# Performance work log

Measured on AMD Instinct MI355X. Metric: run time of the kernel, lower is better.

Reference implementation:

```python
import jax, jax.numpy as jnp
import numpy as np

B, L, D, H = 2, 2048, 1024, 16
HD = D // H
EPS = 1e-6

def _rms(x, w):
    return x * jax.lax.rsqrt(jnp.mean(x * x, axis=-1, keepdims=True) + EPS) * w

def _lin(x, w, b=None):
    y = x @ w.T
    return y if b is None else y + b

def setup_inputs() -> dict:
    key = jax.random.key(0)
    ks = jax.random.split(key, 16)
    def w(i, shape, s=0.02):
        return jax.random.normal(ks[i], shape, dtype=jnp.float32) * s
    return dict(
        z=jax.random.normal(ks[0], (B, L, D), dtype=jnp.float32),
        connection=jax.random.normal(ks[1], (B, L, D), dtype=jnp.float32),
        w_z=jnp.ones(D, jnp.float32), w_c=jnp.ones(D, jnp.float32), w_mlp=jnp.ones(D, jnp.float32),
        f_w1=w(2, (2 * D, D)), f_b1=jnp.zeros(2 * D, jnp.float32),
        f_w2=w(3, (D, 2 * D)), f_b2=jnp.zeros(D, jnp.float32),
        g_w1=w(4, (D, 2 * D)), g_b1=jnp.zeros(D, jnp.float32),
        g_w2=w(5, (D, D)), g_b2=jnp.zeros(D, jnp.float32),
        dt=jnp.float32(0.1),
        q_w=w(6, (D, 2 * D)), k_w=w(7, (D, 2 * D)), v_w=w(8, (D, D)), o_w=w(9, (D, D)),
        temp=jnp.float32(1.0),
        cu_w1=w(10, (2 * D, 3 * D)), cu_b1=jnp.zeros(2 * D, jnp.float32),
        cu_w2=w(11, (D, 2 * D)), cu_b2=jnp.zeros(D, jnp.float32),
        m_w1=w(12, (4 * D, D)), m_b1=jnp.zeros(4 * D, jnp.float32),
        m_w2=w(13, (D, 4 * D)), m_b2=jnp.zeros(D, jnp.float32),
    )

def reference(z, connection, w_z, w_c, w_mlp,
              f_w1, f_b1, f_w2, f_b2, g_w1, g_b1, g_w2, g_b2, dt,
              q_w, k_w, v_w, o_w, temp,
              cu_w1, cu_b1, cu_w2, cu_b2,
              m_w1, m_b1, m_w2, m_b2):
    z_before = z
    zn = _rms(z, w_z)
    cn = _rms(connection, w_c)

    # covariant vector field: dz = dt * (F(zn) + gamma(cat(cn, F(zn))))
    dz_local = _lin(jax.nn.silu(_lin(zn, f_w1, f_b1)), f_w2, f_b2)
    corr = _lin(jnp.tanh(_lin(jnp.concatenate([cn, dz_local], -1), g_w1, g_b1)), g_w2, g_b2)
    dz = dt * (dz_local + corr)

    # covariant sigmoid attention
    zc = jnp.concatenate([zn, cn], -1)                       # [B,L,2D]
    Q = _lin(zc, q_w).reshape(B, L, H, HD).transpose(0, 2, 1, 3)  # bhld
    K = _lin(zc, k_w).reshape(B, L, H, HD).transpose(0, 2, 1, 3)
    V = _lin(zn, v_w).reshape(B, L, H, HD).transpose(0, 2, 1, 3)
    scores = jnp.einsum('bhld,bhmd->bhlm', Q, K) * (HD ** -0.5) * temp
    rel = jax.nn.sigmoid(scores)
    rel_sum = jnp.clip(jnp.sum(rel, -1, keepdims=True), 1.0, None)
    attn = jnp.einsum('bhlm,bhmd->bhld', rel, V) / rel_sum
    ctx = _lin(attn.transpose(0, 2, 1, 3).reshape(B, L, D), o_w)

    z1 = z + dz + ctx

    # connection update
    delta = _lin(jax.nn.silu(_lin(jnp.concatenate([connection, z1, dz], -1), cu_w1, cu_b1)), cu_w2, cu_b2)
    conn_new = connection + delta

    # MLP block
    z2 = z1 + _lin(jax.nn.silu(_lin(_rms(z1, w_mlp), m_w1, m_b1)), m_w2, m_b2)
    return (z2, conn_new, z_before)
```

## Files before the change

### kernel.cpp

```cpp
#include <hip/hip_runtime.h>


typedef unsigned short u16;
typedef __attribute__((ext_vector_type(8))) short short8;
typedef __attribute__((ext_vector_type(8))) unsigned short us8;
typedef __attribute__((ext_vector_type(4))) float f32x4;
typedef __attribute__((ext_vector_type(4))) unsigned short us4;
typedef __attribute__((ext_vector_type(2))) unsigned int u32x2;

__device__ __forceinline__ float b2f(u16 u) {
    union { unsigned u; float f; } c; c.u = ((unsigned)u) << 16; return c.f;
}
__device__ __forceinline__ u16 f2b(float f) {
    union { float f; unsigned u; } c; c.f = f;
    unsigned x = c.u;
    unsigned r = (x + 0x7fffu + ((x >> 16) & 1u)) >> 16;
    return (u16)r;
}
__device__ __forceinline__ float fast_rcp(float x) {
    return __builtin_amdgcn_rcpf(x);
}
__device__ __forceinline__ unsigned cvt_pk_bf16(float a, float b) {
    unsigned r;
    asm("v_cvt_pk_bf16_f32 %0, %1, %2" : "=v"(r) : "v"(a), "v"(b));
    return r;
}

__device__ __forceinline__ void async_copy16(const u16* g, u16* l) {
    __builtin_amdgcn_global_load_lds(
        (const __attribute__((address_space(1))) unsigned int*)(g),
        (__attribute__((address_space(3))) unsigned int*)(l), 16, 0, 0);
}

__global__ __launch_bounds__(256) void cvt_k(const float* __restrict__ s,
                                             u16* __restrict__ d, int n) {
    int i = (blockIdx.x * 256 + threadIdx.x) * 4;
    if (i >= n) return;
    f32x4 v = *(const f32x4*)(s + i);
    us4 o;
#pragma unroll
    for (int k = 0; k < 4; k++) o[k] = f2b(v[k]);
    *(us4*)(d + i) = o;
}

__global__ __launch_bounds__(256) void rmsf_k(const float* __restrict__ x,
                                              const float* __restrict__ w,
                                              u16* __restrict__ y,
                                              float* __restrict__ cp,
                                              u16* __restrict__ cb, int D) {
    int n = blockIdx.x;
    const float* xr = x + (size_t)n * D;
    int i0 = threadIdx.x << 2;
    f32x4 v = *(const f32x4*)(xr + i0);
    if (cp) *(f32x4*)(cp + (size_t)n * D + i0) = v;
    if (cb) {
        us4 o2;
#pragma unroll
        for (int k = 0; k < 4; k++) o2[k] = f2b(v[k]);
        *(us4*)(cb + (size_t)n * D + i0) = o2;
    }
    float s = v[0] * v[0] + v[1] * v[1] + v[2] * v[2] + v[3] * v[3];
#pragma unroll
    for (int m = 32; m >= 1; m >>= 1) s += __shfl_xor(s, m, 64);
    __shared__ float red[4];
    if ((threadIdx.x & 63) == 0) red[threadIdx.x >> 6] = s;
    __syncthreads();
    float tot = red[0] + red[1] + red[2] + red[3];
    float scale = rsqrtf(tot / (float)D + 1e-6f);
    f32x4 wv = *(const f32x4*)(w + i0);
    us4 o;
#pragma unroll
    for (int k = 0; k < 4; k++) o[k] = f2b(v[k] * scale * wv[k]);
    *(us4*)(y + (size_t)n * D + i0) = o;
}

__global__ __launch_bounds__(256) void rmsb_k(const u16* __restrict__ x,
                                              const float* __restrict__ w,
                                              u16* __restrict__ y, int D) {
    int n = blockIdx.x;
    const u16* xr = x + (size_t)n * D;
    int i0 = threadIdx.x << 2;
    us4 xv = *(const us4*)(xr + i0);
    float v[4]; float s = 0.f;
#pragma unroll
    for (int k = 0; k < 4; k++) { v[k] = b2f(xv[k]); s += v[k] * v[k]; }
#pragma unroll
    for (int m = 32; m >= 1; m >>= 1) s += __shfl_xor(s, m, 64);
    __shared__ float red[4];
    if ((threadIdx.x & 63) == 0) red[threadIdx.x >> 6] = s;
    __syncthreads();
    float tot = red[0] + red[1] + red[2] + red[3];
    float scale = rsqrtf(tot / (float)D + 1e-6f);
    f32x4 wv = *(const f32x4*)(w + i0);
    us4 o;
#pragma unroll
    for (int k = 0; k < 4; k++) o[k] = f2b(v[k] * scale * wv[k]);
    *(us4*)(y + (size_t)n * D + i0) = o;
}

template <int BM, int BN, int NSEG>
__global__ __launch_bounds__(256) void gemm_t(const u16* __restrict__ A0,
                                              const u16* __restrict__ A1,
                                              const u16* __restrict__ A2,
                                              const u16* __restrict__ W,
                                              const float* __restrict__ bias,
                                              u16* __restrict__ C,
                                              const u16* __restrict__ Eb,
                                              const float* __restrict__ Ef,
                                              const float* __restrict__ sc,
                                              float* __restrict__ Cf,
                                              int K, int O, int act, int mode) {
    constexpr int WM = BM / 2, WN = BN / 2;
    constexpr int NI = WM / 16, NJ = WN / 16;
    __shared__ u16 Asm[2][BM * 64];
    __shared__ u16 Bsm[2][BN * 64];

    const int tid = threadIdx.x;
    const int wid = tid >> 6, lane = tid & 63;
    const int l15 = lane & 15, quad = lane >> 4;
    const int lsw = l15 & 7;

    const int nwg = gridDim.x * gridDim.y;
    int id = blockIdx.y * gridDim.x + blockIdx.x;
    id = (id & 7) * (nwg >> 3) + (id >> 3);
    const int bx = id % gridDim.x, by = id / gridDim.x;

    const int row0 = by * BM, col0 = bx * BN;
    const int wm = (wid >> 1) * WM, wn = (wid & 1) * WN;

    const int rb = tid >> 3;
    const int gg = ((tid & 7) ^ (rb & 7)) << 3;
    const int sA = (NSEG == 1) ? K : 1024;
    const size_t aoff = (size_t)(row0 + rb) * sA + gg;
    const size_t boff = (size_t)(col0 + rb) * K + gg;
    const int ldsb = wid << 9;

    f32x4 acc[NI][NJ];
#pragma unroll
    for (int i = 0; i < NI; i++)
#pragma unroll
        for (int j = 0; j < NJ; j++) acc[i][j] = (f32x4){0.f, 0.f, 0.f, 0.f};

    auto stage = [&](int buf, int kof) {
        const u16* Ab; int kcol;
        if constexpr (NSEG == 1) { Ab = A0; kcol = kof; }
        else {
            int seg = kof >> 10;
            Ab = (seg == 0) ? A0 : ((NSEG == 3 && seg == 2) ? A2 : A1);
            kcol = kof & 1023;
        }
        const u16* as = Ab + aoff + kcol;
        const u16* bs = W + boff + kof;
#pragma unroll
        for (int i = 0; i < BM / 32; i++)
            async_copy16(as + (size_t)(32 * i) * sA, &Asm[buf][(i << 11) + ldsb]);
#pragma unroll
        for (int i = 0; i < BN / 32; i++)
            async_copy16(bs + (size_t)(32 * i) * K, &Bsm[buf][(i << 11) + ldsb]);
    };

    const int nk = K >> 6;
    stage(0, 0);
    __syncthreads();
    for (int kk = 0; kk < nk; kk++) {
        int cur = kk & 1;
        if (kk + 1 < nk) stage(1 - cur, (kk + 1) << 6);
        const u16* Ab = Asm[cur];
        const u16* Bb = Bsm[cur];
#pragma unroll
        for (int h = 0; h < 2; h++) {
            const int gq = (((h << 2) + quad) ^ lsw) << 3;
            short8 af[NI], bf[NJ];
#pragma unroll
            for (int i = 0; i < NI; i++)
                af[i] = *(const short8*)&Ab[(wm + i * 16 + l15) * 64 + gq];
#pragma unroll
            for (int j = 0; j < NJ; j++)
                bf[j] = *(const short8*)&Bb[(wn + j * 16 + l15) * 64 + gq];
#pragma unroll
            for (int i = 0; i < NI; i++)
#pragma unroll
                for (int j = 0; j < NJ; j++)
                    acc[i][j] = __builtin_amdgcn_mfma_f32_16x16x32_bf16(af[i], bf[j], acc[i][j], 0, 0, 0);
        }
        __syncthreads();
    }

    if (mode == 1) {
#pragma unroll
        for (int j = 0; j < NJ; j++) {
            int col = col0 + wn + j * 16 + l15;
            int h = col >> 6, d = col & 63;
#pragma unroll
            for (int i = 0; i < NI; i++) {
                int rowb = row0 + wm + i * 16 + (quad << 2);
                int bb_ = rowb >> 11;
                int tok = rowb & 2047;
                u32x2 pk2;
                pk2[0] = cvt_pk_bf16(acc[i][j][0], acc[i][j][1]);
                pk2[1] = cvt_pk_bf16(acc[i][j][2], acc[i][j][3]);
                *(u32x2*)&C[(size_t)(((bb_ << 4) + h) * 64 + d) * 2048 + tok] = pk2;
            }
        }
    } else {
        float dtv = (mode == 2) ? sc[0] : 0.f;
#pragma unroll
        for (int j = 0; j < NJ; j++) {
            int col = col0 + wn + j * 16 + l15;
            float bb = bias ? bias[col] : 0.f;
#pragma unroll
            for (int i = 0; i < NI; i++) {
                int rowb = row0 + wm + i * 16 + (quad << 2);
#pragma unroll
                for (int g = 0; g < 4; g++) {
                    float v = acc[i][j][g] + bb;
                    if (act == 1) {
                        v = v * fast_rcp(1.f + __expf(-v));
                    } else if (act == 2) {
                        float t = __expf(v * 2.f);
                        v = 1.f - 2.f * fast_rcp(1.f + t);
                    }
                    size_t idx = (size_t)(rowb + g) * O + col;
                    if (mode == 0)      C[idx] = f2b(v);
                    else if (mode == 2) C[idx] = f2b(dtv * (b2f(Eb[idx]) + v));
                    else if (mode == 3) C[idx] = f2b(Ef[idx] + b2f(Eb[idx]) + v);
                    else if (mode == 4) Cf[idx] = Ef[idx] + v;
                    else                Cf[idx] = b2f(Eb[idx]) + v;
                }
            }
        }
    }
}

__global__ __launch_bounds__(256) void attn_k(const u16* __restrict__ QK,
                                              const u16* __restrict__ VT,
                                              const float* __restrict__ temp_p,
                                              u16* __restrict__ Oa) {
    const int L = 2048, D = 1024, SQ = 2048;
    __shared__ u16 Ks[2][64 * 64];
    __shared__ u16 Vs[2][64 * 64];
    __shared__ u16 plds[4][16 * 72];

    const int tid = threadIdx.x;
    const int w = tid >> 6, lane = tid & 63;
    const int l15 = lane & 15, quad = lane >> 4;
    int id = blockIdx.x;
    id = (id & 7) * 64 + (id >> 3);
    const int bh = id >> 4;
    const int qb0 = (id & 15) << 7;
    const int b = bh >> 4, h = bh & 15;
    const float nsc2 = -0.125f * temp_p[0] * 1.44269504f;

    short8 aq[2][2];
#pragma unroll
    for (int qt = 0; qt < 2; qt++) {
        size_t row = (size_t)(b * L + qb0 + w * 32 + qt * 16 + l15) * SQ + h * 64;
#pragma unroll
        for (int hf = 0; hf < 2; hf++)
            aq[qt][hf] = *(const short8*)(QK + row + hf * 32 + quad * 8);
    }

    const u16* Kbase = QK + 1024 + (size_t)(b * L) * SQ + h * 64;
    const u16* VTb   = VT + (size_t)bh * 64 * L;

    const int i0 = tid, i1 = tid + 256;
    const int r0 = i0 >> 3, g0 = (i0 & 7) ^ (r0 & 7);
    const int r1 = i1 >> 3, g1 = (i1 & 7) ^ (r1 & 7);
    const u16* kS0 = Kbase + (size_t)r0 * SQ + g0 * 8;
    const u16* kS1 = Kbase + (size_t)r1 * SQ + g1 * 8;
    const u16* vS0 = VTb + (size_t)r0 * L + g0 * 8;
    const u16* vS1 = VTb + (size_t)r1 * L + g1 * 8;

    auto stage = [&](int buf, int mc) {
        async_copy16(kS0 + (size_t)mc * SQ, &Ks[buf][w << 9]);
        async_copy16(kS1 + (size_t)mc * SQ, &Ks[buf][2048 + (w << 9)]);
        async_copy16(vS0 + mc, &Vs[buf][w << 9]);
        async_copy16(vS1 + mc, &Vs[buf][2048 + (w << 9)]);
    };

    f32x4 acc[2][4];
#pragma unroll
    for (int i = 0; i < 2; i++)
#pragma unroll
        for (int j = 0; j < 4; j++) acc[i][j] = (f32x4){0.f, 0.f, 0.f, 0.f};
    float rs[2] = {0.f, 0.f};
    u16* P = plds[w];
    const int lsw = l15 & 7;

    stage(0, 0);
    __syncthreads();
    for (int it = 0; it < 32; it++) {
        int cur = it & 1;
        if (it < 31) stage(1 - cur, (it + 1) << 6);
        const u16* Kt = Ks[cur];
        const u16* Vt = Vs[cur];
#pragma unroll
        for (int qt = 0; qt < 2; qt++) {
#pragma unroll
            for (int ks = 0; ks < 4; ks++) {
                f32x4 s = (f32x4){0.f, 0.f, 0.f, 0.f};
#pragma unroll
                for (int hf = 0; hf < 2; hf++) {
                    int slot = ((ks * 16 + l15) * 8 + ((hf * 4 + quad) ^ lsw)) * 8;
                    short8 bk = *(const short8*)&Kt[slot];
                    s = __builtin_amdgcn_mfma_f32_16x16x32_bf16(bk, aq[qt][hf], s, 0, 0, 0);
                }
                float p0 = fast_rcp(1.f + __builtin_amdgcn_exp2f(s[0] * nsc2));
                float p1 = fast_rcp(1.f + __builtin_amdgcn_exp2f(s[1] * nsc2));
                float p2 = fast_rcp(1.f + __builtin_amdgcn_exp2f(s[2] * nsc2));
                float p3 = fast_rcp(1.f + __builtin_amdgcn_exp2f(s[3] * nsc2));
                rs[qt] += (p0 + p1) + (p2 + p3);
                u32x2 pk2;
                pk2[0] = cvt_pk_bf16(p0, p1);
                pk2[1] = cvt_pk_bf16(p2, p3);
                *(u32x2*)&P[l15 * 72 + ks * 16 + (quad << 2)] = pk2;
            }
#pragma unroll
            for (int kh = 0; kh < 2; kh++) {
                short8 ap = *(const short8*)&P[l15 * 72 + kh * 32 + quad * 8];
#pragma unroll
                for (int dt = 0; dt < 4; dt++) {
                    int slot = ((dt * 16 + l15) * 8 + ((kh * 4 + quad) ^ lsw)) * 8;
                    short8 bv = *(const short8*)&Vt[slot];
                    acc[qt][dt] = __builtin_amdgcn_mfma_f32_16x16x32_bf16(ap, bv, acc[qt][dt], 0, 0, 0);
                }
            }
        }
        __syncthreads();
    }

#pragma unroll
    for (int qt = 0; qt < 2; qt++) {
        rs[qt] += __shfl_xor(rs[qt], 16, 64);
        rs[qt] += __shfl_xor(rs[qt], 32, 64);
    }

#pragma unroll
    for (int qt = 0; qt < 2; qt++) {
        u16* orow = Oa + (size_t)(b * L + qb0 + w * 32 + qt * 16) * D + h * 64;
#pragma unroll
        for (int g = 0; g < 4; g++) {
            int row = quad * 4 + g;
            float denom = __shfl(rs[qt], row, 64);
            float rd = fast_rcp(fmaxf(denom, 1.0f));
#pragma unroll
            for (int dt = 0; dt < 4; dt++)
                orow[(size_t)row * D + dt * 16 + l15] = f2b(acc[qt][dt][g] * rd);
        }
    }
}

extern "C" void kernel_launch(void* const* d_in, const int* in_sizes, int n_in,
                              void* d_out, int out_size, void* d_ws, size_t ws_size,
                              hipStream_t stream) {
    const int B = 2, L = 2048, D = 1024, H = 16, N = B * L;
    const float* z      = (const float*)d_in[0];
    const float* conn   = (const float*)d_in[1];
    const float* w_z    = (const float*)d_in[2];
    const float* w_c    = (const float*)d_in[3];
    const float* w_mlp  = (const float*)d_in[4];
    const float* f_w1   = (const float*)d_in[5];
    const float* f_b1   = (const float*)d_in[6];
    const float* f_w2   = (const float*)d_in[7];
    const float* f_b2   = (const float*)d_in[8];
    const float* g_w1   = (const float*)d_in[9];
    const float* g_b1   = (const float*)d_in[10];
    const float* g_w2   = (const float*)d_in[11];
    const float* g_b2   = (const float*)d_in[12];
    const float* dt_p   = (const float*)d_in[13];
    const float* q_w    = (const float*)d_in[14];
    const float* k_w    = (const float*)d_in[15];
    const float* v_w    = (const float*)d_in[16];
    const float* o_w    = (const float*)d_in[17];
    const float* temp_p = (const float*)d_in[18];
    const float* cu_w1  = (const float*)d_in[19];
    const float* cu_b1  = (const float*)d_in[20];
    const float* cu_w2  = (const float*)d_in[21];
    const float* cu_b2  = (const float*)d_in[22];
    const float* m_w1   = (const float*)d_in[23];
    const float* m_b1   = (const float*)d_in[24];
    const float* m_w2   = (const float*)d_in[25];
    const float* m_b2   = (const float*)d_in[26];

    float* out = (float*)d_out;
    u16* ws  = (u16*)d_ws;
    const size_t U = (size_t)N * D;

    u16* zn    = ws + 0 * U;
    u16* cn    = ws + 1 * U;
    u16* h1    = ws + 2 * U;
    u16* dzl   = ws + 4 * U;
    u16* gh    = ws + 5 * U;
    u16* dz    = ws + 6 * U;
    u16* connb = ws + 7 * U;
    u16* QK    = ws + 2 * U;
    u16* VT    = ws + 4 * U;
    u16* attnb = ws + 1 * U;
    u16* z1    = ws + 5 * U;
    u16* cu_h  = ws + 2 * U;
    u16* z1n   = ws + 0 * U;
    u16* mh    = ws + 1 * U;

    u16* wb = ws + 9 * U;
    u16* bf_w1  = wb + 0;
    u16* bf_w2  = wb + 2 * 1024 * 1024;
    u16* bg_w1  = wb + 4 * 1024 * 1024;
    u16* bg_w2  = wb + 6 * 1024 * 1024;
    u16* bqk_w  = wb + 7 * 1024 * 1024;
    u16* bv_w   = wb + 11 * 1024 * 1024;
    u16* bo_w   = wb + 12 * 1024 * 1024;
    u16* bcu_w1 = wb + 13 * 1024 * 1024;
    u16* bcu_w2 = wb + 19 * 1024 * 1024;
    u16* bm_w1  = wb + 21 * 1024 * 1024;
    u16* bm_w2  = wb + 25 * 1024 * 1024;

    auto cvt = [&](const float* s, u16* d, int n) {
        cvt_k<<<n / 1024, 256, 0, stream>>>(s, d, n);
    };
    cvt(f_w1, bf_w1, 2 * D * D);   cvt(f_w2, bf_w2, 2 * D * D);
    cvt(g_w1, bg_w1, 2 * D * D);   cvt(g_w2, bg_w2, D * D);
    cvt(q_w, bqk_w, 2 * D * D);    cvt(k_w, bqk_w + 2 * D * D, 2 * D * D);
    cvt(v_w, bv_w, D * D);         cvt(o_w, bo_w, D * D);
    cvt(cu_w1, bcu_w1, 6 * D * D); cvt(cu_w2, bcu_w2, 2 * D * D);
    cvt(m_w1, bm_w1, 4 * D * D);   cvt(m_w2, bm_w2, 4 * D * D);

    rmsf_k<<<N, 256, 0, stream>>>(z, w_z, zn, out + 2 * U, nullptr, D);
    rmsf_k<<<N, 256, 0, stream>>>(conn, w_c, cn, nullptr, connb, D);

    const u16* nu = nullptr;
    gemm_t<128, 128, 1><<<dim3(16, 32), 256, 0, stream>>>(
        zn, nu, nu, bf_w1, f_b1, h1, nu, nullptr, nullptr, nullptr, D, 2 * D, 1, 0);
    gemm_t<128, 64, 1><<<dim3(16, 32), 256, 0, stream>>>(
        h1, nu, nu, bf_w2, f_b2, dzl, nu, nullptr, nullptr, nullptr, 2 * D, D, 0, 0);
    gemm_t<128, 64, 2><<<dim3(16, 32), 256, 0, stream>>>(
        cn, dzl, nu, bg_w1, g_b1, gh, nu, nullptr, nullptr, nullptr, 2 * D, D, 2, 0);
    gemm_t<128, 64, 1><<<dim3(16, 32), 256, 0, stream>>>(
        gh, nu, nu, bg_w2, g_b2, dz, dzl, nullptr, dt_p, nullptr, D, D, 0, 2);

    gemm_t<128, 128, 2><<<dim3(16, 32), 256, 0, stream>>>(
        zn, cn, nu, bqk_w, nullptr, QK, nu, nullptr, nullptr, nullptr, 2 * D, 2 * D, 0, 0);
    gemm_t<128, 64, 1><<<dim3(16, 32), 256, 0, stream>>>(
        zn, nu, nu, bv_w, nullptr, VT, nu, nullptr, nullptr, nullptr, D, D, 0, 1);
    attn_k<<<B * H * L / 128, 256, 0, stream>>>(QK, VT, temp_p, attnb);
    gemm_t<128, 64, 1><<<dim3(16, 32), 256, 0, stream>>>(
        attnb, nu, nu, bo_w, nullptr, z1, dz, z, nullptr, nullptr, D, D, 0, 3);

    gemm_t<128, 128, 3><<<dim3(16, 32), 256, 0, stream>>>(
        connb, z1, dz, bcu_w1, cu_b1, cu_h, nu, nullptr, nullptr, nullptr, 3 * D, 2 * D, 1, 0);
    gemm_t<128, 64, 1><<<dim3(16, 32), 256, 0, stream>>>(
        cu_h, nu, nu, bcu_w2, cu_b2, (u16*)nullptr, nu, conn, nullptr, out + U, 2 * D, D, 0, 4);

    rmsb_k<<<N, 256, 0, stream>>>(z1, w_mlp, z1n, D);
    gemm_t<128, 128, 1><<<dim3(32, 32), 256, 0, stream>>>(
        z1n, nu, nu, bm_w1, m_b1, mh, nu, nullptr, nullptr, nullptr, D, 4 * D, 1, 0);
    gemm_t<128, 64, 1><<<dim3(16, 32), 256, 0, stream>>>(
        mh, nu, nu, bm_w2, m_b2, (u16*)nullptr, z1, nullptr, nullptr, out, 4 * D, D, 0, 5);
}
```

Measured before the change: 741.6 us.

## Merge weight conversions into one launch and halve attention query tile

The twelve fp32-to-bf16 weight conversion launches become a single kernel that finds each block's segment from a cumulative block table. The attention kernel now handles 64 queries per block (16 per wave) instead of 128, so it launches twice as many blocks. This should cut launch overhead and give the attention kernel more parallelism and fewer registers per wave. In exchange, each K/V tile staged in shared memory is reused by half as many queries, which doubles K/V load traffic.

After: 728.4 us. About the same (-1.8%).

```diff
diff --git a/kernel.cpp b/kernel.cpp
--- a/kernel.cpp
+++ b/kernel.cpp
@@ -32,10 +32,18 @@
         (__attribute__((address_space(3))) unsigned int*)(l), 16, 0, 0);
 }
 
-__global__ __launch_bounds__(256) void cvt_k(const float* __restrict__ s,
-                                             u16* __restrict__ d, int n) {
-    int i = (blockIdx.x * 256 + threadIdx.x) * 4;
-    if (i >= n) return;
+struct CvtArgs {
+    const float* s[12];
+    int cum[13];
+};
+__global__ __launch_bounds__(256) void cvtall_k(CvtArgs a, u16* __restrict__ dst) {
+    int blk = blockIdx.x;
+    int seg = 0;
+    while (blk >= a.cum[seg + 1]) seg++;
+    int local = blk - a.cum[seg];
+    const float* s = a.s[seg] + (size_t)local * 1024;
+    u16* d = dst + (size_t)blk * 1024;
+    int i = threadIdx.x << 2;
     f32x4 v = *(const f32x4*)(s + i);
     us4 o;
 #pragma unroll
@@ -245,19 +253,18 @@
     const int w = tid >> 6, lane = tid & 63;
     const int l15 = lane & 15, quad = lane >> 4;
     int id = blockIdx.x;
-    id = (id & 7) * 64 + (id >> 3);
-    const int bh = id >> 4;
-    const int qb0 = (id & 15) << 7;
+    id = (id & 7) * 128 + (id >> 3);
+    const int bh = id >> 5;
+    const int qb0 = (id & 31) << 6;
     const int b = bh >> 4, h = bh & 15;
     const float nsc2 = -0.125f * temp_p[0] * 1.44269504f;
 
-    short8 aq[2][2];
-#pragma unroll
-    for (int qt = 0; qt < 2; qt++) {
-        size_t row = (size_t)(b * L + qb0 + w * 32 + qt * 16 + l15) * SQ + h * 64;
+    short8 aq[2];
+    {
+        size_t row = (size_t)(b * L + qb0 + w * 16 + l15) * SQ + h * 64;
 #pragma unroll
         for (int hf = 0; hf < 2; hf++)
-            aq[qt][hf] = *(const short8*)(QK + row + hf * 32 + quad * 8);
+            aq[hf] = *(const short8*)(QK + row + hf * 32 + quad * 8);
     }
 
     const u16* Kbase = QK + 1024 + (size_t)(b * L) * SQ + h * 64;
@@ -278,12 +285,10 @@
         async_copy16(vS1 + mc, &Vs[buf][2048 + (w << 9)]);
     };
 
-    f32x4 acc[2][4];
-#pragma unroll
-    for (int i = 0; i < 2; i++)
-#pragma unroll
-        for (int j = 0; j < 4; j++) acc[i][j] = (f32x4){0.f, 0.f, 0.f, 0.f};
-    float rs[2] = {0.f, 0.f};
+    f32x4 acc[4];
+#pragma unroll
+    for (int j = 0; j < 4; j++) acc[j] = (f32x4){0.f, 0.f, 0.f, 0.f};
+    float rs = 0.f;
     u16* P = plds[w];
     const int lsw = l15 & 7;
 
@@ -295,58 +300,49 @@
         const u16* Kt = Ks[cur];
         const u16* Vt = Vs[cur];
 #pragma unroll
-        for (int qt = 0; qt < 2; qt++) {
-#pragma unroll
-            for (int ks = 0; ks < 4; ks++) {
-                f32x4 s = (f32x4){0.f, 0.f, 0.f, 0.f};
-#pragma unroll
-                for (int hf = 0; hf < 2; hf++) {
-                    int slot = ((ks * 16 + l15) * 8 + ((hf * 4 + quad) ^ lsw)) * 8;
-                    short8 bk = *(const short8*)&Kt[slot];
-                    s = __builtin_amdgcn_mfma_f32_16x16x32_bf16(bk, aq[qt][hf], s, 0, 0, 0);
-                }
-                float p0 = fast_rcp(1.f + __builtin_amdgcn_exp2f(s[0] * nsc2));
-                float p1 = fast_rcp(1.f + __builtin_amdgcn_exp2f(s[1] * nsc2));
-                float p2 = fast_rcp(1.f + __builtin_amdgcn_exp2f(s[2] * nsc2));
-                float p3 = fast_rcp(1.f + __builtin_amdgcn_exp2f(s[3] * nsc2));
-                rs[qt] += (p0 + p1) + (p2 + p3);
-                u32x2 pk2;
-                pk2[0] = cvt_pk_bf16(p0, p1);
-                pk2[1] = cvt_pk_bf16(p2, p3);
-                *(u32x2*)&P[l15 * 72 + ks * 16 + (quad << 2)] = pk2;
+        for (int ks = 0; ks < 4; ks++) {
+            f32x4 s = (f32x4){0.f, 0.f, 0.f, 0.f};
+#pragma unroll
+            for (int hf = 0; hf < 2; hf++) {
+                int slot = ((ks * 16 + l15) * 8 + ((hf * 4 + quad) ^ lsw)) * 8;
+                short8 bk = *(const short8*)&Kt[slot];
+                s = __builtin_amdgcn_mfma_f32_16x16x32_bf16(bk, aq[hf], s, 0, 0, 0);
             }
-#pragma unroll
-            for (int kh = 0; kh < 2; kh++) {
-                short8 ap = *(const short8*)&P[l15 * 72 + kh * 32 + quad * 8];
-#pragma unroll
-                for (int dt = 0; dt < 4; dt++) {
-                    int slot = ((dt * 16 + l15) * 8 + ((kh * 4 + quad) ^ lsw)) * 8;
-                    short8 bv = *(const short8*)&Vt[slot];
-                    acc[qt][dt] = __builtin_amdgcn_mfma_f32_16x16x32_bf16(ap, bv, acc[qt][dt], 0, 0, 0);
-                }
+            float p0 = fast_rcp(1.f + __builtin_amdgcn_exp2f(s[0] * nsc2));
+            float p1 = fast_rcp(1.f + __builtin_amdgcn_exp2f(s[1] * nsc2));
+            float p2 = fast_rcp(1.f + __builtin_amdgcn_exp2f(s[2] * nsc2));
+            float p3 = fast_rcp(1.f + __builtin_amdgcn_exp2f(s[3] * nsc2));
+            rs += (p0 + p1) + (p2 + p3);
+            u32x2 pk2;
+            pk2[0] = cvt_pk_bf16(p0, p1);
+            pk2[1] = cvt_pk_bf16(p2, p3);
+            *(u32x2*)&P[l15 * 72 + ks * 16 + (quad << 2)] = pk2;
+        }
+#pragma unroll
+        for (int kh = 0; kh < 2; kh++) {
+            short8 ap = *(const short8*)&P[l15 * 72 + kh * 32 + quad * 8];
+#pragma unroll
+            for (int dt = 0; dt < 4; dt++) {
+                int slot = ((dt * 16 + l15) * 8 + ((kh * 4 + quad) ^ lsw)) * 8;
+                short8 bv = *(const short8*)&Vt[slot];
+                acc[dt] = __builtin_amdgcn_mfma_f32_16x16x32_bf16(ap, bv, acc[dt], 0, 0, 0);
             }
         }
         __syncthreads();
     }
 
-#pragma unroll
-    for (int qt = 0; qt < 2; qt++) {
-        rs[qt] += __shfl_xor(rs[qt], 16, 64);
-        rs[qt] += __shfl_xor(rs[qt], 32, 64);
-    }
-
-#pragma unroll
-    for (int qt = 0; qt < 2; qt++) {
-        u16* orow = Oa + (size_t)(b * L + qb0 + w * 32 + qt * 16) * D + h * 64;
-#pragma unroll
-        for (int g = 0; g < 4; g++) {
-            int row = quad * 4 + g;
-            float denom = __shfl(rs[qt], row, 64);
-            float rd = fast_rcp(fmaxf(denom, 1.0f));
-#pragma unroll
-            for (int dt = 0; dt < 4; dt++)
-                orow[(size_t)row * D + dt * 16 + l15] = f2b(acc[qt][dt][g] * rd);
-        }
+    rs += __shfl_xor(rs, 16, 64);
+    rs += __shfl_xor(rs, 32, 64);
+
+    u16* orow = Oa + (size_t)(b * L + qb0 + w * 16) * D + h * 64;
+#pragma unroll
+    for (int g = 0; g < 4; g++) {
+        int row = quad * 4 + g;
+        float denom = __shfl(rs, row, 64);
+        float rd = fast_rcp(fmaxf(denom, 1.0f));
+#pragma unroll
+        for (int dt = 0; dt < 4; dt++)
+            orow[(size_t)row * D + dt * 16 + l15] = f2b(acc[dt][g] * rd);
     }
 }
 
@@ -414,15 +410,15 @@
     u16* bm_w1  = wb + 21 * 1024 * 1024;
     u16* bm_w2  = wb + 25 * 1024 * 1024;
 
-    auto cvt = [&](const float* s, u16* d, int n) {
-        cvt_k<<<n / 1024, 256, 0, stream>>>(s, d, n);
-    };
-    cvt(f_w1, bf_w1, 2 * D * D);   cvt(f_w2, bf_w2, 2 * D * D);
-    cvt(g_w1, bg_w1, 2 * D * D);   cvt(g_w2, bg_w2, D * D);
-    cvt(q_w, bqk_w, 2 * D * D);    cvt(k_w, bqk_w + 2 * D * D, 2 * D * D);
-    cvt(v_w, bv_w, D * D);         cvt(o_w, bo_w, D * D);
-    cvt(cu_w1, bcu_w1, 6 * D * D); cvt(cu_w2, bcu_w2, 2 * D * D);
-    cvt(m_w1, bm_w1, 4 * D * D);   cvt(m_w2, bm_w2, 4 * D * D);
+    CvtArgs ca;
+    ca.s[0] = f_w1;  ca.s[1] = f_w2;  ca.s[2] = g_w1;  ca.s[3] = g_w2;
+    ca.s[4] = q_w;   ca.s[5] = k_w;   ca.s[6] = v_w;   ca.s[7] = o_w;
+    ca.s[8] = cu_w1; ca.s[9] = cu_w2; ca.s[10] = m_w1; ca.s[11] = m_w2;
+    const int segb[12] = {2048, 2048, 2048, 1024, 2048, 2048, 1024, 1024,
+                          6144, 2048, 4096, 4096};
+    ca.cum[0] = 0;
+    for (int i = 0; i < 12; i++) ca.cum[i + 1] = ca.cum[i] + segb[i];
+    cvtall_k<<<ca.cum[12], 256, 0, stream>>>(ca, wb);
 
     rmsf_k<<<N, 256, 0, stream>>>(z, w_z, zn, out + 2 * U, nullptr, D);
     rmsf_k<<<N, 256, 0, stream>>>(conn, w_c, cn, nullptr, connb, D);
@@ -441,7 +437,7 @@
         zn, cn, nu, bqk_w, nullptr, QK, nu, nullptr, nullptr, nullptr, 2 * D, 2 * D, 0, 0);
     gemm_t<128, 64, 1><<<dim3(16, 32), 256, 0, stream>>>(
         zn, nu, nu, bv_w, nullptr, VT, nu, nullptr, nullptr, nullptr, D, D, 0, 1);
-    attn_k<<<B * H * L / 128, 256, 0, stream>>>(QK, VT, temp_p, attnb);
+    attn_k<<<B * H * L / 64, 256, 0, stream>>>(QK, VT, temp_p, attnb);
     gemm_t<128, 64, 1><<<dim3(16, 32), 256, 0, stream>>>(
         attnb, nu, nu, bo_w, nullptr, z1, dz, z, nullptr, nullptr, D, D, 0, 3);
 
```
